# Kernel optimization log

Hardware: AMD Instinct MI355X
Metric: run time of the kernel (lower is better)

The kernel has to match this reference:

```python
import jax, jax.numpy as jnp
import numpy as np

FEATURE_DIM = 256
NUM_HEADS = 8
HEAD_DIM = FEATURE_DIM // NUM_HEADS
LOCAL_RADIUS = 3.0
N_CUR = 4096
N_HIST = 4096
COORD_EXTENT = 16.0


def setup_inputs() -> dict:
    key = jax.random.key(0)
    ks = jax.random.split(key, 12)
    s = 1.0 / np.sqrt(FEATURE_DIM)  # ~nn.Linear init scale
    return {
        "current_feats": jax.random.normal(ks[0], (N_CUR, FEATURE_DIM), jnp.float32),
        "historical_feats": jax.random.normal(ks[1], (N_HIST, FEATURE_DIM), jnp.float32),
        "current_coords": jax.random.uniform(ks[2], (N_CUR, 3), jnp.float32) * COORD_EXTENT,
        "historical_coords": jax.random.uniform(ks[3], (N_HIST, 3), jnp.float32) * COORD_EXTENT,
        "Wq": jax.random.normal(ks[4], (FEATURE_DIM, FEATURE_DIM), jnp.float32) * s,
        "bq": jnp.zeros((FEATURE_DIM,), jnp.float32),
        "Wk": jax.random.normal(ks[5], (FEATURE_DIM, FEATURE_DIM), jnp.float32) * s,
        "bk": jnp.zeros((FEATURE_DIM,), jnp.float32),
        "Wv": jax.random.normal(ks[6], (FEATURE_DIM, FEATURE_DIM), jnp.float32) * s,
        "bv": jnp.zeros((FEATURE_DIM,), jnp.float32),
        "Wo": jax.random.normal(ks[7], (FEATURE_DIM, FEATURE_DIM), jnp.float32) * s,
        "bo": jnp.zeros((FEATURE_DIM,), jnp.float32),
    }


def reference(current_feats, historical_feats, current_coords, historical_coords,
              Wq, bq, Wk, bk, Wv, bv, Wo, bo):
    # local mask: squared distance <= radius^2 (identical to norm <= radius)
    diff = current_coords[:, None, :] - historical_coords[None, :, :]  # [Nq, Nk, 3]
    local_mask = jnp.sum(diff * diff, axis=-1) <= LOCAL_RADIUS ** 2      # [Nq, Nk]

    q = (current_feats @ Wq.T + bq).reshape(N_CUR, NUM_HEADS, HEAD_DIM)
    k = (historical_feats @ Wk.T + bk).reshape(N_HIST, NUM_HEADS, HEAD_DIM)
    v = (historical_feats @ Wv.T + bv).reshape(N_HIST, NUM_HEADS, HEAD_DIM)

    scores = jnp.einsum('qhd,khd->qhk', q, k) / np.sqrt(HEAD_DIM)        # [Nq, H, Nk]
    scores = jnp.where(local_mask[:, None, :], scores, -jnp.inf)
    attn = jax.nn.softmax(scores, axis=-1)  # dropout is identity in eval
    out = jnp.einsum('qhk,khd->qhd', attn, v).reshape(N_CUR, FEATURE_DIM)
    return out @ Wo.T + bo
```

## Files before the change

### kernel.cpp

```cpp
#include <hip/hip_runtime.h>
#include <math.h>

#define FDIM 256
#define NH 8
#define HD 32
#define NQ 4096
#define NKEY 4096
#define CAP 512
#define R2 9.0f

typedef _Float16 half8 __attribute__((ext_vector_type(8)));
typedef _Float16 half4v __attribute__((ext_vector_type(4)));
typedef float f32x4 __attribute__((ext_vector_type(4)));
typedef unsigned short ushort_t;

#define CB_CUR  0
#define CB_HIST 1048576
#define CB_WQ   2097152
#define CB_WK   2162688
#define CB_WV   2228224
#define CB_WO   2293760
#define CB_F4_TOTAL 589824

__global__ __launch_bounds__(256) void prep(const float* __restrict__ cur,
                                            const float* __restrict__ hist,
                                            const float* __restrict__ Wq,
                                            const float* __restrict__ Wk,
                                            const float* __restrict__ Wv,
                                            const float* __restrict__ Wo,
                                            _Float16* __restrict__ dst,
                                            const float* __restrict__ qc,
                                            const float* __restrict__ kc,
                                            ushort_t* __restrict__ nbr,
                                            int* __restrict__ cnt) {
    if (blockIdx.x < 1024) {
        const int q    = blockIdx.x * 4 + (threadIdx.x >> 6);
        const int lane = threadIdx.x & 63;
        const float qx = qc[q * 3 + 0];
        const float qy = qc[q * 3 + 1];
        const float qz = qc[q * 3 + 2];
        int base = 0;
        for (int k0 = 0; k0 < NKEY; k0 += 64) {
            const int k = k0 + lane;
            float dx = __fsub_rn(qx, kc[k * 3 + 0]);
            float dy = __fsub_rn(qy, kc[k * 3 + 1]);
            float dz = __fsub_rn(qz, kc[k * 3 + 2]);
            float d2 = __fadd_rn(__fadd_rn(__fmul_rn(dx, dx), __fmul_rn(dy, dy)),
                                 __fmul_rn(dz, dz));
            bool valid = (d2 <= R2);
            unsigned long long bal = __ballot(valid);
            if (valid) {
                int pos = base + __popcll(bal & ((1ull << lane) - 1ull));
                if (pos < CAP) nbr[(size_t)q * CAP + pos] = (ushort_t)k;
            }
            base += __popcll(bal);
        }
        if (lane == 0) cnt[q] = (base > CAP) ? CAP : base;
    } else {
        const int stride = 1024 * 256;
        for (int i4 = (blockIdx.x - 1024) * 256 + threadIdx.x; i4 < CB_F4_TOTAL;
             i4 += stride) {
            const float* src;
            int base;
            if (i4 < 262144)      { src = cur;  base = 0; }
            else if (i4 < 524288) { src = hist; base = 262144; }
            else if (i4 < 540672) { src = Wq;   base = 524288; }
            else if (i4 < 557056) { src = Wk;   base = 540672; }
            else if (i4 < 573440) { src = Wv;   base = 557056; }
            else                  { src = Wo;   base = 573440; }
            float4 v = ((const float4*)src)[i4 - base];
            half4v h;
            h[0] = (_Float16)v.x; h[1] = (_Float16)v.y;
            h[2] = (_Float16)v.z; h[3] = (_Float16)v.w;
            ((half4v*)dst)[i4] = h;
        }
    }
}

__device__ __forceinline__ void mfma_tile_16x64(const _Float16* __restrict__ A,
                                                const _Float16* __restrict__ W,
                                                int m0, int n0, int wave, int lane,
                                                f32x4 acc[4]) {
    const int row  = lane & 15;
    const int quad = lane >> 4;
    const _Float16* aptr = A + (size_t)(m0 + wave * 16 + row) * 256 + quad * 8;
    const _Float16* wptr = W + (size_t)(n0 + row) * 256 + quad * 8;
#pragma unroll
    for (int i = 0; i < 4; ++i) acc[i] = (f32x4){0.f, 0.f, 0.f, 0.f};
#pragma unroll
    for (int k0 = 0; k0 < 8; ++k0) {
        half8 a = *(const half8*)(aptr + k0 * 32);
#pragma unroll
        for (int nt = 0; nt < 4; ++nt) {
            half8 b = *(const half8*)(wptr + (size_t)nt * 16 * 256 + k0 * 32);
            acc[nt] = __builtin_amdgcn_mfma_f32_16x16x32_f16(a, b, acc[nt], 0, 0, 0);
        }
    }
}

__global__ __launch_bounds__(256) void qkv_mfma(const _Float16* __restrict__ cb,
                                                const float* __restrict__ bq,
                                                const float* __restrict__ bk,
                                                const float* __restrict__ bv,
                                                _Float16* __restrict__ Qh,
                                                _Float16* __restrict__ KV) {
    const int z    = blockIdx.z;
    const int wave = threadIdx.x >> 6;
    const int lane = threadIdx.x & 63;
    const int m0   = blockIdx.y * 64;
    const int n0   = blockIdx.x * 64;

    const _Float16* A = (z == 0) ? (cb + CB_CUR) : (cb + CB_HIST);
    const _Float16* W = (z == 0) ? (cb + CB_WQ) : (z == 1) ? (cb + CB_WK) : (cb + CB_WV);
    const float* bias = (z == 0) ? bq : (z == 1) ? bk : bv;

    f32x4 acc[4];
    mfma_tile_16x64(A, W, m0, n0, wave, lane, acc);

    const int col  = lane & 15;
    const int quad = lane >> 4;
    float bs[4];
#pragma unroll
    for (int nt = 0; nt < 4; ++nt) bs[nt] = bias[n0 + nt * 16 + col];

    if (z == 0) {
#pragma unroll
        for (int nt = 0; nt < 4; ++nt)
#pragma unroll
            for (int r = 0; r < 4; ++r)
                Qh[(size_t)(m0 + wave * 16 + quad * 4 + r) * 256 + n0 + nt * 16 + col] =
                    (_Float16)(acc[nt][r] + bs[nt]);
    } else {
        const int off = (z == 1) ? 0 : 256;
#pragma unroll
        for (int nt = 0; nt < 4; ++nt)
#pragma unroll
            for (int r = 0; r < 4; ++r)
                KV[(size_t)(m0 + wave * 16 + quad * 4 + r) * 512 + off + n0 + nt * 16 + col] =
                    (_Float16)(acc[nt][r] + bs[nt]);
    }
}

__global__ __launch_bounds__(256) void o_mfma(const _Float16* __restrict__ Ob,
                                              const _Float16* __restrict__ Wo,
                                              const float* __restrict__ bo,
                                              float* __restrict__ out) {
    const int wave = threadIdx.x >> 6;
    const int lane = threadIdx.x & 63;
    const int m0   = blockIdx.y * 64;
    const int n0   = blockIdx.x * 64;

    f32x4 acc[4];
    mfma_tile_16x64(Ob, Wo, m0, n0, wave, lane, acc);

    const int col  = lane & 15;
    const int quad = lane >> 4;
#pragma unroll
    for (int nt = 0; nt < 4; ++nt) {
        const float b = bo[n0 + nt * 16 + col];
#pragma unroll
        for (int r = 0; r < 4; ++r)
            out[(size_t)(m0 + wave * 16 + quad * 4 + r) * 256 + n0 + nt * 16 + col] =
                acc[nt][r] + b;
    }
}

__global__ __launch_bounds__(256) void sparse_attn9(const _Float16* __restrict__ Qh,
                                                    const _Float16* __restrict__ KV,
                                                    const ushort_t* __restrict__ nbr,
                                                    const int* __restrict__ cnt,
                                                    _Float16* __restrict__ Ob) {
    __shared__ float sm[4][32][12];
    const int q    = blockIdx.x;
    const int t    = threadIdx.x;
    const int wave = t >> 6;
    const int lane = t & 63;
    const int p    = lane >> 5;
    const int h    = (lane >> 2) & 7;
    const int s    = lane & 3;

    float qv[8];
    {
        half8 qh = *(const half8*)(Qh + (size_t)q * FDIM + h * HD + s * 8);
        const float sc = 0.17677669529663687f;
#pragma unroll
        for (int i = 0; i < 8; ++i) qv[i] = (float)qh[i] * sc;
    }

    float o[8];
#pragma unroll
    for (int i = 0; i < 8; ++i) o[i] = 0.f;
    float l = 0.f;

    const int n = cnt[q];
    const ushort_t* nl = nbr + (size_t)q * CAP;
    const int koff = h * HD + s * 8;

    for (int j = 2 * wave + p; j < n; j += 8) {
        const int k = nl[j];
        const _Float16* r = KV + ((size_t)k << 9) + koff;
        half8 k8 = *(const half8*)(r);
        half8 v8 = *(const half8*)(r + 256);

        float part = 0.f;
#pragma unroll
        for (int i = 0; i < 8; ++i)
            part = fmaf(qv[i], (float)k8[i], part);
        part += __shfl_xor(part, 1, 64);
        part += __shfl_xor(part, 2, 64);

        const float pw = __expf(part);
        l += pw;
#pragma unroll
        for (int i = 0; i < 8; ++i)
            o[i] = fmaf(pw, (float)v8[i], o[i]);
    }

    l += __shfl_xor(l, 32, 64);
#pragma unroll
    for (int i = 0; i < 8; ++i) o[i] += __shfl_xor(o[i], 32, 64);

    if (lane < 32) {
        float* dst = &sm[wave][lane][0];
        *(float4*)(dst)     = (float4){o[0], o[1], o[2], o[3]};
        *(float4*)(dst + 4) = (float4){o[4], o[5], o[6], o[7]};
        dst[8] = l;
    }
    __syncthreads();

    if (t < 32) {
        float4 x0 = *(const float4*)&sm[0][t][0];
        float4 x1 = *(const float4*)&sm[0][t][4];
        float O[8] = {x0.x, x0.y, x0.z, x0.w, x1.x, x1.y, x1.z, x1.w};
        float L = sm[0][t][8];
#pragma unroll
        for (int w = 1; w < 4; ++w) {
            float4 y0 = *(const float4*)&sm[w][t][0];
            float4 y1 = *(const float4*)&sm[w][t][4];
            L += sm[w][t][8];
            O[0] += y0.x; O[1] += y0.y; O[2] += y0.z; O[3] += y0.w;
            O[4] += y1.x; O[5] += y1.y; O[6] += y1.z; O[7] += y1.w;
        }
        const float inv = 1.0f / L;
        half8 ho;
#pragma unroll
        for (int i = 0; i < 8; ++i) ho[i] = (_Float16)(O[i] * inv);
        *(half8*)(Ob + (size_t)q * FDIM + t * 8) = ho;
    }
}

extern "C" void kernel_launch(void* const* d_in, const int* in_sizes, int n_in,
                              void* d_out, int out_size, void* d_ws, size_t ws_size,
                              hipStream_t stream) {
    const float* cur_feats   = (const float*)d_in[0];
    const float* hist_feats  = (const float*)d_in[1];
    const float* cur_coords  = (const float*)d_in[2];
    const float* hist_coords = (const float*)d_in[3];
    const float* bq = (const float*)d_in[5];
    const float* bk = (const float*)d_in[7];
    const float* bv = (const float*)d_in[9];
    const float* bo = (const float*)d_in[11];
    float* out = (float*)d_out;

    char* w = (char*)d_ws;
    _Float16*  Qh   = (_Float16*)(w);
    _Float16*  KV   = (_Float16*)(w + (4 << 20));
    ushort_t*  nbr  = (ushort_t*)(w + (8 << 20));
    int*       cnt  = (int*)(w + (12 << 20));
    _Float16*  Ob   = (_Float16*)(w + (12 << 20) + (64 << 10));
    _Float16*  cb   = (_Float16*)(w + (15 << 20));

    prep<<<2048, 256, 0, stream>>>(cur_feats, hist_feats,
                                   (const float*)d_in[4], (const float*)d_in[6],
                                   (const float*)d_in[8], (const float*)d_in[10], cb,
                                   cur_coords, hist_coords, nbr, cnt);

    qkv_mfma<<<dim3(4, 64, 3), 256, 0, stream>>>(cb, bq, bk, bv, Qh, KV);

    sparse_attn9<<<NQ, 256, 0, stream>>>(Qh, KV, nbr, cnt, Ob);

    o_mfma<<<dim3(4, 64), 256, 0, stream>>>(Ob, cb + CB_WO, bo, out);
}
```

Baseline: 145.7 us.

## Reorder attention queries by spatial cell and use nontemporal loads/stores

Adds an extra prep block that buckets queries into a 4x4x4 Morton-ordered spatial grid and writes a permutation. The attention kernel maps each block to a query from that order, with an XCD-aware swizzle of the block index, so that spatially close queries, which gather overlapping K/V rows, run on the same L2. Streaming accesses (Q row, neighbor list, output) now use nontemporal hints so they do not evict K/V from cache. The cost is one extra serial single-block histogram/scatter inside prep, plus the indirection through the order array.

```diff
diff --git a/kernel.cpp b/kernel.cpp
--- a/kernel.cpp
+++ b/kernel.cpp
@@ -12,6 +12,7 @@
 typedef _Float16 half8 __attribute__((ext_vector_type(8)));
 typedef _Float16 half4v __attribute__((ext_vector_type(4)));
 typedef float f32x4 __attribute__((ext_vector_type(4)));
+typedef unsigned int u32x4 __attribute__((ext_vector_type(4)));
 typedef unsigned short ushort_t;
 
 #define CB_CUR  0
@@ -22,8 +23,30 @@
 #define CB_WO   2293760
 #define CB_F4_TOTAL 589824
 
+__device__ __forceinline__ half8 nt_load_half8(const _Float16* p) {
+    u32x4 u = __builtin_nontemporal_load((const u32x4*)p);
+    union { u32x4 u; half8 h; } c; c.u = u; return c.h;
+}
+__device__ __forceinline__ void nt_store_half8(_Float16* p, half8 h) {
+    union { u32x4 u; half8 h; } c; c.h = h;
+    __builtin_nontemporal_store(c.u, (u32x4*)p);
+}
+
+__device__ __forceinline__ int cell_id(float x, float y, float z) {
+    int cx = (int)(x * 0.25f); cx = cx < 0 ? 0 : (cx > 3 ? 3 : cx);
+    int cy = (int)(y * 0.25f); cy = cy < 0 ? 0 : (cy > 3 ? 3 : cy);
+    int cz = (int)(z * 0.25f); cz = cz < 0 ? 0 : (cz > 3 ? 3 : cz);
+    int m = 0;
+#pragma unroll
+    for (int b = 0; b < 2; ++b)
+        m |= (((cx >> b) & 1) << (3 * b + 2)) |
+             (((cy >> b) & 1) << (3 * b + 1)) |
+             (((cz >> b) & 1) << (3 * b + 0));
+    return m;
+}
+
 __global__ __launch_bounds__(256) void prep(const float* __restrict__ cur,
-                                            const float* __restrict__ hist,
+                                            const float* __restrict__ histf,
                                             const float* __restrict__ Wq,
                                             const float* __restrict__ Wk,
                                             const float* __restrict__ Wv,
@@ -32,7 +55,8 @@
                                             const float* __restrict__ qc,
                                             const float* __restrict__ kc,
                                             ushort_t* __restrict__ nbr,
-                                            int* __restrict__ cnt) {
+                                            int* __restrict__ cnt,
+                                            ushort_t* __restrict__ order) {
     if (blockIdx.x < 1024) {
         const int q    = blockIdx.x * 4 + (threadIdx.x >> 6);
         const int lane = threadIdx.x & 63;
@@ -56,23 +80,45 @@
             base += __popcll(bal);
         }
         if (lane == 0) cnt[q] = (base > CAP) ? CAP : base;
-    } else {
+    } else if (blockIdx.x < 2048) {
         const int stride = 1024 * 256;
         for (int i4 = (blockIdx.x - 1024) * 256 + threadIdx.x; i4 < CB_F4_TOTAL;
              i4 += stride) {
             const float* src;
             int base;
-            if (i4 < 262144)      { src = cur;  base = 0; }
-            else if (i4 < 524288) { src = hist; base = 262144; }
-            else if (i4 < 540672) { src = Wq;   base = 524288; }
-            else if (i4 < 557056) { src = Wk;   base = 540672; }
-            else if (i4 < 573440) { src = Wv;   base = 557056; }
-            else                  { src = Wo;   base = 573440; }
+            if (i4 < 262144)      { src = cur;   base = 0; }
+            else if (i4 < 524288) { src = histf; base = 262144; }
+            else if (i4 < 540672) { src = Wq;    base = 524288; }
+            else if (i4 < 557056) { src = Wk;    base = 540672; }
+            else if (i4 < 573440) { src = Wv;    base = 557056; }
+            else                  { src = Wo;    base = 573440; }
             float4 v = ((const float4*)src)[i4 - base];
             half4v h;
             h[0] = (_Float16)v.x; h[1] = (_Float16)v.y;
             h[2] = (_Float16)v.z; h[3] = (_Float16)v.w;
             ((half4v*)dst)[i4] = h;
+        }
+    } else {
+        __shared__ int hcell[64];
+        __shared__ int hoff[64];
+        const int t = threadIdx.x;
+        if (t < 64) hcell[t] = 0;
+        __syncthreads();
+        for (int q = t; q < NQ; q += 256) {
+            int c = cell_id(qc[q * 3 + 0], qc[q * 3 + 1], qc[q * 3 + 2]);
+            atomicAdd(&hcell[c], 1);
+        }
+        __syncthreads();
+        if (t == 0) {
+            int s = 0;
+#pragma unroll
+            for (int i = 0; i < 64; ++i) { hoff[i] = s; s += hcell[i]; }
+        }
+        __syncthreads();
+        for (int q = t; q < NQ; q += 256) {
+            int c = cell_id(qc[q * 3 + 0], qc[q * 3 + 1], qc[q * 3 + 2]);
+            int pos = atomicAdd(&hoff[c], 1);
+            order[pos] = (ushort_t)q;
         }
     }
 }
@@ -165,13 +211,16 @@
     }
 }
 
-__global__ __launch_bounds__(256) void sparse_attn9(const _Float16* __restrict__ Qh,
-                                                    const _Float16* __restrict__ KV,
-                                                    const ushort_t* __restrict__ nbr,
-                                                    const int* __restrict__ cnt,
-                                                    _Float16* __restrict__ Ob) {
+__global__ __launch_bounds__(256) void sparse_attn10(const _Float16* __restrict__ Qh,
+                                                     const _Float16* __restrict__ KV,
+                                                     const ushort_t* __restrict__ nbr,
+                                                     const int* __restrict__ cnt,
+                                                     const ushort_t* __restrict__ order,
+                                                     _Float16* __restrict__ Ob) {
     __shared__ float sm[4][32][12];
-    const int q    = blockIdx.x;
+    const int b    = blockIdx.x;
+    const int widx = ((b & 7) << 9) | (b >> 3);
+    const int q    = (int)order[widx];
     const int t    = threadIdx.x;
     const int wave = t >> 6;
     const int lane = t & 63;
@@ -181,7 +230,7 @@
 
     float qv[8];
     {
-        half8 qh = *(const half8*)(Qh + (size_t)q * FDIM + h * HD + s * 8);
+        half8 qh = nt_load_half8(Qh + (size_t)q * FDIM + h * HD + s * 8);
         const float sc = 0.17677669529663687f;
 #pragma unroll
         for (int i = 0; i < 8; ++i) qv[i] = (float)qh[i] * sc;
@@ -197,7 +246,7 @@
     const int koff = h * HD + s * 8;
 
     for (int j = 2 * wave + p; j < n; j += 8) {
-        const int k = nl[j];
+        const int k = (int)__builtin_nontemporal_load(nl + j);
         const _Float16* r = KV + ((size_t)k << 9) + koff;
         half8 k8 = *(const half8*)(r);
         half8 v8 = *(const half8*)(r + 256);
@@ -245,7 +294,7 @@
         half8 ho;
 #pragma unroll
         for (int i = 0; i < 8; ++i) ho[i] = (_Float16)(O[i] * inv);
-        *(half8*)(Ob + (size_t)q * FDIM + t * 8) = ho;
+        nt_store_half8(Ob + (size_t)q * FDIM + t * 8, ho);
     }
 }
 
@@ -263,21 +312,22 @@
     float* out = (float*)d_out;
 
     char* w = (char*)d_ws;
-    _Float16*  Qh   = (_Float16*)(w);
-    _Float16*  KV   = (_Float16*)(w + (4 << 20));
-    ushort_t*  nbr  = (ushort_t*)(w + (8 << 20));
-    int*       cnt  = (int*)(w + (12 << 20));
-    _Float16*  Ob   = (_Float16*)(w + (12 << 20) + (64 << 10));
-    _Float16*  cb   = (_Float16*)(w + (15 << 20));
-
-    prep<<<2048, 256, 0, stream>>>(cur_feats, hist_feats,
+    _Float16*  Qh    = (_Float16*)(w);
+    _Float16*  KV    = (_Float16*)(w + (4 << 20));
+    ushort_t*  nbr   = (ushort_t*)(w + (8 << 20));
+    int*       cnt   = (int*)(w + (12 << 20));
+    ushort_t*  order = (ushort_t*)(w + (12 << 20) + (32 << 10));
+    _Float16*  Ob    = (_Float16*)(w + (12 << 20) + (64 << 10));
+    _Float16*  cb    = (_Float16*)(w + (15 << 20));
+
+    prep<<<2049, 256, 0, stream>>>(cur_feats, hist_feats,
                                    (const float*)d_in[4], (const float*)d_in[6],
                                    (const float*)d_in[8], (const float*)d_in[10], cb,
-                                   cur_coords, hist_coords, nbr, cnt);
+                                   cur_coords, hist_coords, nbr, cnt, order);
 
     qkv_mfma<<<dim3(4, 64, 3), 256, 0, stream>>>(cb, bq, bk, bv, Qh, KV);
 
-    sparse_attn9<<<NQ, 256, 0, stream>>>(Qh, KV, nbr, cnt, Ob);
+    sparse_attn10<<<NQ, 256, 0, stream>>>(Qh, KV, nbr, cnt, order, Ob);
 
     o_mfma<<<dim3(4, 64), 256, 0, stream>>>(Ob, cb + CB_WO, bo, out);
 }
```

Measured after the change: 147.2 us. No clear change (+1.0%).
